# Performance work log

Measured on AMD Instinct MI355X. Metric: run time of the kernel, lower is better.

Reference implementation:

```python
import jax, jax.numpy as jnp
import numpy as np

A, R = 180, 180  # numAngle, numRho
EPS = 1e-5


def _hough_seg_ids(H, W):
    # Deep Hough Transform binning (Hanqer/deep-hough-transform initTab):
    # irho = int(sqrt(H^2+W^2)+1)/(numRho-1); theta_k = k*pi/numAngle
    irho = int(np.sqrt(H * H + W * W) + 1) / float(R - 1)
    theta = np.arange(A) * (np.pi / A)
    tab_cos = np.cos(theta) / irho  # [A]
    tab_sin = np.sin(theta) / irho
    xs = np.arange(W) - W // 2  # x is width index
    ys = np.arange(H) - H // 2
    r = np.round(tab_cos[:, None, None] * xs[None, None, :]
                 + tab_sin[:, None, None] * ys[None, :, None]).astype(np.int64) + R // 2
    r = np.clip(r, 0, R - 1)
    return jnp.asarray(r.reshape(A, H * W))  # [A, H*W] rho-bin per (angle, pixel)


def _conv_bn_relu(x, w, b, g, beta, m, v, pad):
    y = jax.lax.conv_general_dilated(
        x, w, window_strides=(1, 1), padding=[(pad, pad), (pad, pad)],
        dimension_numbers=('NCHW', 'OIHW', 'NCHW'))
    y = y + b[None, :, None, None]
    scale = g / jnp.sqrt(v + EPS)
    y = (y - m[None, :, None, None]) * scale[None, :, None, None] + beta[None, :, None, None]
    return jax.nn.relu(y)


def _dht(f):
    # f: [N, C, H, W] -> accum [N, C, A, R]
    N, C, H, W = f.shape
    seg = _hough_seg_ids(H, W)  # [A, HW]
    ft = f.reshape(N, C, H * W).transpose(2, 0, 1).reshape(H * W, N * C)  # [HW, N*C]
    acc = jax.vmap(lambda s: jax.ops.segment_sum(ft, s, num_segments=R))(seg)  # [A, R, N*C]
    return acc.reshape(A, R, N, C).transpose(2, 3, 0, 1)  # [N, C, A, R]


def setup_inputs() -> dict:
    key = jax.random.key(0)
    ks = jax.random.split(key, 24)
    N, Ci, dim, H, W = 8, 256, 128, 128, 128
    inp = {
        'x': jax.random.normal(ks[0], (N, Ci, H, W), jnp.float32),
        'w1': jax.random.normal(ks[1], (dim, Ci, 1, 1), jnp.float32) * (1.0 / np.sqrt(Ci)),
        'b1': jax.random.normal(ks[2], (dim,), jnp.float32) * 0.01,
        'g1': jax.random.uniform(ks[3], (dim,), jnp.float32, 0.5, 1.5),
        'be1': jax.random.normal(ks[4], (dim,), jnp.float32) * 0.01,
        'm1': jax.random.normal(ks[5], (dim,), jnp.float32) * 0.1,
        'v1': jax.random.uniform(ks[6], (dim,), jnp.float32, 0.5, 1.5),
        'w2': jax.random.normal(ks[7], (dim, dim, 3, 3), jnp.float32) * (1.0 / np.sqrt(dim * 9)),
        'b2': jax.random.normal(ks[8], (dim,), jnp.float32) * 0.01,
        'g2': jax.random.uniform(ks[9], (dim,), jnp.float32, 0.5, 1.5),
        'be2': jax.random.normal(ks[10], (dim,), jnp.float32) * 0.01,
        'm2': jax.random.normal(ks[11], (dim,), jnp.float32) * 0.1,
        'v2': jax.random.uniform(ks[12], (dim,), jnp.float32, 0.5, 1.5),
        'w3': jax.random.normal(ks[13], (dim, dim, 3, 3), jnp.float32) * (1.0 / np.sqrt(dim * 9)),
        'b3': jax.random.normal(ks[14], (dim,), jnp.float32) * 0.01,
        'g3': jax.random.uniform(ks[15], (dim,), jnp.float32, 0.5, 1.5),
        'be3': jax.random.normal(ks[16], (dim,), jnp.float32) * 0.01,
        'm3': jax.random.normal(ks[17], (dim,), jnp.float32) * 0.1,
        'v3': jax.random.uniform(ks[18], (dim,), jnp.float32, 0.5, 1.5),
    }
    return inp


def reference(x, w1, b1, g1, be1, m1, v1,
              w2, b2, g2, be2, m2, v2,
              w3, b3, g3, be3, m3, v3):
    f = _conv_bn_relu(x, w1, b1, g1, be1, m1, v1, pad=0)   # 1x1 conv + BN + ReLU
    acc = _dht(f)                                           # [N, dim, A, R]
    y = _conv_bn_relu(acc, w2, b2, g2, be2, m2, v2, pad=1)  # 3x3 conv + BN + ReLU
    y = _conv_bn_relu(y, w3, b3, g3, be3, m3, v3, pad=1)
    return y
```

## Files before the change

### kernel.cpp

```cpp
#include <hip/hip_runtime.h>
#include <hip/hip_bf16.h>
#include <math.h>

#define NB 8
#define CI 256
#define CD 128
#define HH 128
#define WW 128
#define HW (HH*WW)
#define AANG 180
#define RRHO 180
#define PADD 182
#define M2 (AANG*RRHO)

typedef __attribute__((ext_vector_type(8))) short short8;
typedef __attribute__((ext_vector_type(8))) _Float16 half8;
typedef __attribute__((ext_vector_type(2))) _Float16 h2;
typedef __attribute__((ext_vector_type(4))) float floatx4;
typedef __attribute__((ext_vector_type(2))) float floatx2;

static __device__ __forceinline__ void async_cp16(const void* g, void* l) {
  __builtin_amdgcn_global_load_lds((const __attribute__((address_space(1))) unsigned int*)g,
                                   (__attribute__((address_space(3))) unsigned int*)l,
                                   16, 0, 0);
}

static __device__ __forceinline__ unsigned short f2bf(float f) {
  unsigned int u = __builtin_bit_cast(unsigned int, f);
  unsigned int r = (u + 0x7fffu + ((u >> 16) & 1u)) >> 16;
  return (unsigned short)r;
}

static __device__ __forceinline__ unsigned short f2h(float f) {
  return __builtin_bit_cast(unsigned short, (_Float16)f);
}

static __device__ __forceinline__ void acc2(float& aL, float& aH, unsigned int u,
                                            h2 eL, h2 eH) {
  h2 hv = __builtin_bit_cast(h2, u);
#if __has_builtin(__builtin_amdgcn_fdot2)
  aL = __builtin_amdgcn_fdot2(hv, eL, aL, false);
  aH = __builtin_amdgcn_fdot2(hv, eH, aH, false);
#else
  aL += (float)hv.x;
  aH += (float)hv.y;
#endif
}

__global__ void prep_kernel(const float* __restrict__ w1, const float* __restrict__ w2,
                            const float* __restrict__ w3,
                            const float* b1, const float* g1, const float* be1,
                            const float* m1, const float* v1,
                            const float* b2, const float* g2, const float* be2,
                            const float* m2, const float* v2,
                            const float* b3, const float* g3, const float* be3,
                            const float* m3, const float* v3,
                            unsigned short* __restrict__ wK1, unsigned short* __restrict__ wK2,
                            unsigned short* __restrict__ wK3,
                            float* __restrict__ sc, float* __restrict__ sh) {
  int idx = blockIdx.x * 256 + threadIdx.x;
  if (idx < 32768) {
    wK1[idx] = f2h(w1[idx]);
  } else if (idx < 32768 + 147456) {
    int i = idx - 32768;
    int co = i / 1152, k = i % 1152;
    int dydx = k >> 7, ci = k & 127;
    int dst = (((dydx*2 + (ci >> 6)) * 128 + co) * 64) + (ci & 63);
    wK2[dst] = f2bf(w2[(size_t)(co*128 + ci)*9 + dydx]);
  } else if (idx < 32768 + 2*147456) {
    int i = idx - 32768 - 147456;
    int co = i / 1152, k = i % 1152;
    int dydx = k >> 7, ci = k & 127;
    int dst = (((dydx*2 + (ci >> 6)) * 128 + co) * 64) + (ci & 63);
    wK3[dst] = f2bf(w3[(size_t)(co*128 + ci)*9 + dydx]);
  } else if (idx < 32768 + 2*147456 + 384) {
    int j = idx - 32768 - 2*147456;
    int c = j >> 7, co = j & 127;
    const float* b  = c==0?b1 :(c==1?b2 :b3);
    const float* g  = c==0?g1 :(c==1?g2 :g3);
    const float* be = c==0?be1:(c==1?be2:be3);
    const float* m  = c==0?m1 :(c==1?m2 :m3);
    const float* v  = c==0?v1 :(c==1?v2 :v3);
    float s = g[co] * rsqrtf(v[co] + 1e-5f);
    sc[c*128 + co] = s;
    sh[c*128 + co] = (b[co] - m[co]) * s + be[co];
  }
}

__global__ void hist_kernel(unsigned char* __restrict__ seg, unsigned int* __restrict__ offs) {
  int a = blockIdx.x, t = threadIdx.x;
  __shared__ unsigned int h[RRHO];
  if (t < RRHO) h[t] = 0;
  __syncthreads();
  double th = (double)a * (M_PI / 180.0);
  double Cc = cos(th) / (182.0 / 179.0);
  double Ss = sin(th) / (182.0 / 179.0);
  for (int p = t; p < HW; p += 256) {
    int x = (p & 127) - 64;
    int y = (p >> 7) - 64;
    int r = (int)rint(Cc * (double)x + Ss * (double)y) + 90;
    r = r < 0 ? 0 : (r > 179 ? 179 : r);
    seg[(size_t)a*HW + p] = (unsigned char)r;
    atomicAdd(&h[r], 1u);
  }
  __syncthreads();
  if (t == 0) {
    unsigned int run = 0;
    for (int r = 0; r < RRHO; ++r) { offs[a*192 + r] = run; run += h[r]; }
    offs[a*192 + RRHO] = run;
  }
}

__global__ void fill_kernel(const unsigned char* __restrict__ seg,
                            const unsigned int* __restrict__ offs,
                            unsigned short* __restrict__ lst16) {
  int a = blockIdx.x, t = threadIdx.x;
  __shared__ unsigned int pos[RRHO];
  if (t < RRHO) pos[t] = offs[a*192 + t];
  __syncthreads();
  int p0 = t * 64;
  for (int i = 0; i < 64; ++i) {
    int p = p0 + i;
    int r = seg[(size_t)a*HW + p];
    unsigned int ix = atomicAdd(&pos[r], 1u);
    lst16[(size_t)a*HW + ix] = (unsigned short)p;
  }
}

__global__ void zero_border(uint4* __restrict__ accP, uint4* __restrict__ y2P,
                            unsigned int* __restrict__ qcnt) {
  int idx = blockIdx.x * 256 + threadIdx.x;
  if (idx < 8) qcnt[idx] = 0;
  if (idx >= NB * PADD * PADD) return;
  int rc = idx % (PADD * PADD);
  int row = rc / PADD, col = rc % PADD;
  if (row != 0 && row != PADD-1 && col != 0 && col != PADD-1) return;
  uint4 z = {0u, 0u, 0u, 0u};
  size_t base = (size_t)idx * 16;
  #pragma unroll
  for (int i = 0; i < 16; ++i) { accP[base + i] = z; y2P[base + i] = z; }
}

__global__ __launch_bounds__(256) void conv1_kernel(
    const float* __restrict__ x, const unsigned short* __restrict__ wK,
    const float* __restrict__ sc, const float* __restrict__ sh,
    unsigned short* __restrict__ f) {
  __shared__ short Al[4*128*8];
  __shared__ short Bl[4*128*8];
  int t = threadIdx.x;
  int m0 = blockIdx.x * 128;
  int n = blockIdx.y;
  int lane = t & 63, wv = t >> 6, wm = wv & 1, wn = wv >> 1;
  int mloc = t & 127, octb = t >> 7;
  floatx4 acc[4][4];
  #pragma unroll
  for (int i = 0; i < 4; ++i)
    #pragma unroll
    for (int j = 0; j < 4; ++j) acc[i][j] = (floatx4){0.f, 0.f, 0.f, 0.f};
  const float* xn = x + (size_t)n * CI * HW;
  for (int kc = 0; kc < 8; ++kc) {
    if (kc) __syncthreads();
    #pragma unroll
    for (int j = 0; j < 2; ++j) {
      int oct = octb + 2*j;
      const float* src = xn + (size_t)(kc*32 + oct*8) * HW + m0 + mloc;
      float v[8];
      #pragma unroll
      for (int e = 0; e < 8; ++e) v[e] = src[(size_t)e * HW];
      uint4 pk;
      pk.x = __builtin_bit_cast(unsigned int, __builtin_amdgcn_cvt_pkrtz(v[0], v[1]));
      pk.y = __builtin_bit_cast(unsigned int, __builtin_amdgcn_cvt_pkrtz(v[2], v[3]));
      pk.z = __builtin_bit_cast(unsigned int, __builtin_amdgcn_cvt_pkrtz(v[4], v[5]));
      pk.w = __builtin_bit_cast(unsigned int, __builtin_amdgcn_cvt_pkrtz(v[6], v[7]));
      *reinterpret_cast<uint4*>(&Al[(size_t)(t + 256*j) * 8]) = pk;
    }
    #pragma unroll
    for (int j = 0; j < 2; ++j) {
      int oct = octb + 2*j;
      async_cp16(wK + (size_t)mloc * 256 + kc*32 + oct*8,
                 &Bl[(size_t)((t & 0xFFC0) + 256*j) * 8]);
    }
    __syncthreads();
    int q = lane >> 4, l15 = lane & 15;
    short8 af[4], bfr[4];
    #pragma unroll
    for (int i = 0; i < 4; ++i)
      af[i] = *reinterpret_cast<const short8*>(&Al[((q*128) + wm*64 + i*16 + l15) * 8]);
    #pragma unroll
    for (int j = 0; j < 4; ++j)
      bfr[j] = *reinterpret_cast<const short8*>(&Bl[((q*128) + wn*64 + j*16 + l15) * 8]);
    #pragma unroll
    for (int i = 0; i < 4; ++i)
      #pragma unroll
      for (int j = 0; j < 4; ++j)
        acc[i][j] = __builtin_amdgcn_mfma_f32_16x16x32_f16(
            __builtin_bit_cast(half8, af[i]), __builtin_bit_cast(half8, bfr[j]),
            acc[i][j], 0, 0, 0);
  }
  int q = lane >> 4, l15 = lane & 15;
  #pragma unroll
  for (int j = 0; j < 4; ++j) {
    int co = wn*64 + j*16 + l15;
    float s = sc[co], hb = sh[co];
    #pragma unroll
    for (int i = 0; i < 4; ++i) {
      #pragma unroll
      for (int rg = 0; rg < 4; ++rg) {
        int m = m0 + wm*64 + i*16 + q*4 + rg;
        float v = acc[i][j][rg] * s + hb;
        v = fmaxf(v, 0.f);
        f[((size_t)n * HW + m) * 128 + co] = f2h(v);
      }
    }
  }
}

__global__ __launch_bounds__(512, 8) void dht_kernel(
    const unsigned short* __restrict__ lst16, const unsigned int* __restrict__ offs,
    const unsigned int* __restrict__ f, unsigned int* __restrict__ accP,
    unsigned int* __restrict__ qcnt) {
  __shared__ unsigned short Ls[HW];
  __shared__ unsigned int Os[RRHO + 1];
  __shared__ int sWork;
  int t = threadIdx.x;
  if (t == 0) {
    unsigned int xcd;
    asm volatile("s_getreg_b32 %0, hwreg(HW_REG_XCC_ID, 0, 32)" : "=s"(xcd));
    xcd &= 7u;
    int work = 0;
    for (int k = 0; k < 8; ++k) {
      unsigned int q = (xcd + (unsigned int)k) & 7u;
      unsigned int tk = atomicAdd(&qcnt[q], 1u);
      if (tk < 360u) { work = (int)(q * 360u + tk); break; }
    }
    sWork = work;
  }
  __syncthreads();
  int work = sWork;
  int n = work / 360;
  int rem = work % 360;
  int h = rem / 180;
  int a = rem % 180;
  {
    const uint4* src = (const uint4*)(lst16 + (size_t)a * HW);
    uint4* dst = (uint4*)Ls;
    if (t < RRHO + 1) Os[t] = offs[a*192 + t];
    #pragma unroll
    for (int i = 0; i < 4; ++i) dst[t + 512*i] = src[t + 512*i];
  }
  __syncthreads();
  int w = t >> 6, lane = t & 63;
  int sub = lane >> 3;
  int co  = lane & 7;
  const char* fb = (const char*)(f + (size_t)n * HW * 64);
  unsigned int loff = (unsigned int)(h*32 + co*4) * 4u;
  const h2 eL = {(_Float16)1.0f, (_Float16)0.0f};
  const h2 eH = {(_Float16)0.0f, (_Float16)1.0f};
  for (int r = w; r < RRHO; r += 8) {
    int o0 = (int)Os[r];
    int cnt = (int)Os[r+1] - o0;
    float accL[4], accH[4];
    #pragma unroll
    for (int j = 0; j < 4; ++j) { accL[j] = 0.f; accH[j] = 0.f; }
    int i = 0;
    for (; i + 32 <= cnt; i += 32) {
      unsigned int p0 = Ls[o0 + i + sub];
      unsigned int p1 = Ls[o0 + i + 8 + sub];
      unsigned int p2 = Ls[o0 + i + 16 + sub];
      unsigned int p3 = Ls[o0 + i + 24 + sub];
      uint4 v0 = *(const uint4*)(fb + ((p0 << 8) + loff));
      uint4 v1 = *(const uint4*)(fb + ((p1 << 8) + loff));
      uint4 v2 = *(const uint4*)(fb + ((p2 << 8) + loff));
      uint4 v3 = *(const uint4*)(fb + ((p3 << 8) + loff));
      const unsigned int u0[4] = {v0.x, v0.y, v0.z, v0.w};
      const unsigned int u1[4] = {v1.x, v1.y, v1.z, v1.w};
      const unsigned int u2[4] = {v2.x, v2.y, v2.z, v2.w};
      const unsigned int u3[4] = {v3.x, v3.y, v3.z, v3.w};
      #pragma unroll
      for (int j = 0; j < 4; ++j) {
        acc2(accL[j], accH[j], u0[j], eL, eH);
        acc2(accL[j], accH[j], u1[j], eL, eH);
        acc2(accL[j], accH[j], u2[j], eL, eH);
        acc2(accL[j], accH[j], u3[j], eL, eH);
      }
    }
    for (; i + 8 <= cnt; i += 8) {
      unsigned int p0 = Ls[o0 + i + sub];
      uint4 v0 = *(const uint4*)(fb + ((p0 << 8) + loff));
      const unsigned int u0[4] = {v0.x, v0.y, v0.z, v0.w};
      #pragma unroll
      for (int j = 0; j < 4; ++j)
        acc2(accL[j], accH[j], u0[j], eL, eH);
    }
    if (i < cnt) {
      int idx = i + sub;
      int cl = idx < cnt ? idx : (cnt - 1);
      unsigned int p0 = Ls[o0 + cl];
      uint4 v0 = *(const uint4*)(fb + ((p0 << 8) + loff));
      unsigned int u0[4] = {v0.x, v0.y, v0.z, v0.w};
      if (idx >= cnt) { u0[0] = 0; u0[1] = 0; u0[2] = 0; u0[3] = 0; }
      #pragma unroll
      for (int j = 0; j < 4; ++j)
        acc2(accL[j], accH[j], u0[j], eL, eH);
    }
    #pragma unroll
    for (int m = 8; m <= 32; m <<= 1) {
      #pragma unroll
      for (int j = 0; j < 4; ++j) {
        accL[j] += __shfl_xor(accL[j], m, 64);
        accH[j] += __shfl_xor(accH[j], m, 64);
      }
    }
    if (sub == 0) {
      uint4 out;
      out.x = (unsigned int)f2bf(accL[0]) | ((unsigned int)f2bf(accH[0]) << 16);
      out.y = (unsigned int)f2bf(accL[1]) | ((unsigned int)f2bf(accH[1]) << 16);
      out.z = (unsigned int)f2bf(accL[2]) | ((unsigned int)f2bf(accH[2]) << 16);
      out.w = (unsigned int)f2bf(accL[3]) | ((unsigned int)f2bf(accH[3]) << 16);
      size_t o = (((size_t)n*PADD + (a+1))*PADD + (r+1))*64 + h*32 + co*4;
      *(uint4*)(accP + o) = out;
    }
  }
}

template<int MODE>
__global__ __launch_bounds__(256) void conv3x3_kernel(
    const unsigned short* __restrict__ inP,
    const unsigned short* __restrict__ wKr,
    const float* __restrict__ sc, const float* __restrict__ sh,
    void* __restrict__ outp) {
  __shared__ short Al[128*64];
  __shared__ short Bl[128*64];
  int t = threadIdx.x;
  int m0 = blockIdx.x * 128;
  int n = blockIdx.y;
  int lane = t & 63, w = t >> 6, wm = w & 1, wn = w >> 1;
  floatx4 acc[4][4];
  #pragma unroll
  for (int i = 0; i < 4; ++i)
    #pragma unroll
    for (int j = 0; j < 4; ++j) acc[i][j] = (floatx4){0.f, 0.f, 0.f, 0.f};

  int srcOct = ((lane & 7) - (lane >> 3)) & 7;
  const unsigned short* rpA[4];
  unsigned int offB[4];
  #pragma unroll
  for (int i = 0; i < 4; ++i) {
    int row = w*32 + i*8 + (lane >> 3);
    int mg = m0 + row; if (mg > M2 - 1) mg = M2 - 1;
    int oa = mg / 180, orr = mg % 180;
    rpA[i] = inP + (((size_t)n*PADD + oa)*PADD + orr)*128 + srcOct*8;
    offB[i] = (unsigned int)(row*64 + srcOct*8);
  }

  for (int step = 0; step < 18; ++step) {
    int dydx = step >> 1, cc2 = step & 1;
    int dy = (dydx * 11) >> 5, dx = dydx - dy*3;
    int doff = (dy*PADD + dx)*128 + cc2*64;
    if (step) __syncthreads();
    #pragma unroll
    for (int i = 0; i < 4; ++i) {
      async_cp16(rpA[i] + doff, &Al[(size_t)((w*4 + i)*64 + lane) * 8]);
      async_cp16(wKr + (size_t)step*8192 + offB[i],
                 &Bl[(size_t)((w*4 + i)*64 + lane) * 8]);
    }
    __syncthreads();
    int q = lane >> 4, l15 = lane & 15;
    #pragma unroll
    for (int kk = 0; kk < 2; ++kk) {
      int o = kk*4 + q;
      int swz = ((o + l15) & 7) * 8;
      short8 rf[4], cf[4];
      #pragma unroll
      for (int i = 0; i < 4; ++i) {
        int addr = (wm*64 + i*16 + l15)*64 + swz;
        rf[i] = *reinterpret_cast<const short8*>(MODE == 1 ? &Al[addr] : &Bl[addr]);
      }
      #pragma unroll
      for (int j = 0; j < 4; ++j) {
        int addr = (wn*64 + j*16 + l15)*64 + swz;
        cf[j] = *reinterpret_cast<const short8*>(MODE == 1 ? &Bl[addr] : &Al[addr]);
      }
      #pragma unroll
      for (int i = 0; i < 4; ++i)
        #pragma unroll
        for (int j = 0; j < 4; ++j)
          acc[i][j] = __builtin_amdgcn_mfma_f32_16x16x32_bf16(rf[i], cf[j], acc[i][j], 0, 0, 0);
    }
  }
  int q = lane >> 4, l15 = lane & 15;
  if (MODE == 1) {
    unsigned short* out = (unsigned short*)outp;
    #pragma unroll
    for (int j = 0; j < 4; ++j) {
      int co = wn*64 + j*16 + l15;
      float s = sc[co], hb = sh[co];
      #pragma unroll
      for (int i = 0; i < 4; ++i) {
        #pragma unroll
        for (int rg = 0; rg < 4; ++rg) {
          int m = m0 + wm*64 + i*16 + q*4 + rg;
          if (m < M2) {
            float v = fmaxf(acc[i][j][rg] * s + hb, 0.f);
            int oa2 = m / 180, or2 = m % 180;
            out[(((size_t)n*PADD + oa2 + 1)*PADD + or2 + 1)*128 + co] = f2bf(v);
          }
        }
      }
    }
  } else {
    float* out = (float*)outp;
    #pragma unroll
    for (int i = 0; i < 4; ++i) {
      #pragma unroll
      for (int rg = 0; rg < 4; ++rg) {
        int co = wm*64 + i*16 + q*4 + rg;
        float s = sc[co], hb = sh[co];
        #pragma unroll
        for (int j = 0; j < 4; ++j) {
          int m = m0 + wn*64 + j*16 + l15;
          if (m < M2) {
            float v = fmaxf(acc[i][j][rg] * s + hb, 0.f);
            out[((size_t)n*128 + co)*M2 + m] = v;
          }
        }
      }
    }
  }
}

extern "C" void kernel_launch(void* const* d_in, const int* in_sizes, int n_in,
                              void* d_out, int out_size, void* d_ws, size_t ws_size,
                              hipStream_t stream) {
  const float* x  = (const float*)d_in[0];
  const float* w1 = (const float*)d_in[1];
  const float* b1 = (const float*)d_in[2];
  const float* g1 = (const float*)d_in[3];
  const float* be1= (const float*)d_in[4];
  const float* m1 = (const float*)d_in[5];
  const float* v1 = (const float*)d_in[6];
  const float* w2 = (const float*)d_in[7];
  const float* b2 = (const float*)d_in[8];
  const float* g2 = (const float*)d_in[9];
  const float* be2= (const float*)d_in[10];
  const float* m2 = (const float*)d_in[11];
  const float* v2 = (const float*)d_in[12];
  const float* w3 = (const float*)d_in[13];
  const float* b3 = (const float*)d_in[14];
  const float* g3 = (const float*)d_in[15];
  const float* be3= (const float*)d_in[16];
  const float* m3 = (const float*)d_in[17];
  const float* v3 = (const float*)d_in[18];

  size_t off = 0;
  char* ws = (char*)d_ws;
  auto alloc = [&](size_t sz) -> void* {
    void* p = ws + off;
    off = (off + sz + 255) & ~(size_t)255;
    return p;
  };
  unsigned short* fbuf = (unsigned short*)alloc((size_t)NB*HW*128*2);
  unsigned short* accP = (unsigned short*)alloc((size_t)NB*PADD*PADD*128*2);
  unsigned short* y2P  = (unsigned short*)alloc((size_t)NB*PADD*PADD*128*2);
  unsigned short* wK1  = (unsigned short*)alloc(32768*2);
  unsigned short* wK2  = (unsigned short*)alloc(147456*2);
  unsigned short* wK3  = (unsigned short*)alloc(147456*2);
  float* sc = (float*)alloc(384*4);
  float* sh = (float*)alloc(384*4);
  unsigned char* seg  = (unsigned char*)alloc((size_t)AANG*HW);
  unsigned int* offs  = (unsigned int*)alloc((size_t)AANG*192*4);
  unsigned short* lst16 = (unsigned short*)alloc((size_t)AANG*HW*2);
  unsigned int* qcnt  = (unsigned int*)alloc(8*4);

  prep_kernel<<<1282, 256, 0, stream>>>(w1, w2, w3,
      b1, g1, be1, m1, v1, b2, g2, be2, m2, v2, b3, g3, be3, m3, v3,
      wK1, wK2, wK3, sc, sh);
  hist_kernel<<<AANG, 256, 0, stream>>>(seg, offs);
  fill_kernel<<<AANG, 256, 0, stream>>>(seg, offs, lst16);
  zero_border<<<(NB*PADD*PADD + 255)/256, 256, 0, stream>>>((uint4*)accP, (uint4*)y2P, qcnt);
  conv1_kernel<<<dim3(HW/128, NB), 256, 0, stream>>>(x, wK1, sc, sh, fbuf);
  dht_kernel<<<NB*AANG*2, 512, 0, stream>>>(lst16, offs, (const unsigned int*)fbuf,
                                            (unsigned int*)accP, qcnt);
  conv3x3_kernel<1><<<dim3((M2 + 127)/128, NB), 256, 0, stream>>>(
      accP, wK2, sc + 128, sh + 128, y2P);
  conv3x3_kernel<2><<<dim3((M2 + 127)/128, NB), 256, 0, stream>>>(
      y2P, wK3, sc + 256, sh + 256, d_out);
}
```

Measured before the change: 747.9 us.

## Double-buffer conv3x3 LDS loads and widen Hough gather unroll

The conv3x3 kernel now double-buffers its A and B tiles in LDS. It issues the async global-to-LDS copy for the next K step before computing the current one, using explicit vmcnt waits and barriers, so load latency overlaps with MFMA work. The Hough gather loop now processes 64 entries per iteration, taking 32 from each end of the segment, to keep more global loads in flight. In exchange, the conv kernel uses twice the LDS (64KB), which may reduce occupancy, and the code depends on hand-written waitcnt counts being correct.

```diff
diff --git a/kernel.cpp b/kernel.cpp
--- a/kernel.cpp
+++ b/kernel.cpp
@@ -45,6 +45,14 @@
   aL += (float)hv.x;
   aH += (float)hv.y;
 #endif
+}
+
+static __device__ __forceinline__ void acc4(float* aL, float* aH, const uint4& v,
+                                            h2 eL, h2 eH) {
+  acc2(aL[0], aH[0], v.x, eL, eH);
+  acc2(aL[1], aH[1], v.y, eL, eH);
+  acc2(aL[2], aH[2], v.z, eL, eH);
+  acc2(aL[3], aH[3], v.w, eL, eH);
 }
 
 __global__ void prep_kernel(const float* __restrict__ w1, const float* __restrict__ w2,
@@ -257,51 +265,58 @@
   const h2 eL = {(_Float16)1.0f, (_Float16)0.0f};
   const h2 eH = {(_Float16)0.0f, (_Float16)1.0f};
   for (int r = w; r < RRHO; r += 8) {
-    int o0 = (int)Os[r];
-    int cnt = (int)Os[r+1] - o0;
+    int lo = (int)Os[r];
+    int hi = (int)Os[r+1];
     float accL[4], accH[4];
     #pragma unroll
     for (int j = 0; j < 4; ++j) { accL[j] = 0.f; accH[j] = 0.f; }
-    int i = 0;
-    for (; i + 32 <= cnt; i += 32) {
-      unsigned int p0 = Ls[o0 + i + sub];
-      unsigned int p1 = Ls[o0 + i + 8 + sub];
-      unsigned int p2 = Ls[o0 + i + 16 + sub];
-      unsigned int p3 = Ls[o0 + i + 24 + sub];
+    while (hi - lo >= 64) {
+      unsigned int p0 = Ls[lo + sub];
+      unsigned int p1 = Ls[lo + 8 + sub];
+      unsigned int p2 = Ls[lo + 16 + sub];
+      unsigned int p3 = Ls[lo + 24 + sub];
+      unsigned int p4 = Ls[hi - 32 + sub];
+      unsigned int p5 = Ls[hi - 24 + sub];
+      unsigned int p6 = Ls[hi - 16 + sub];
+      unsigned int p7 = Ls[hi - 8 + sub];
       uint4 v0 = *(const uint4*)(fb + ((p0 << 8) + loff));
       uint4 v1 = *(const uint4*)(fb + ((p1 << 8) + loff));
       uint4 v2 = *(const uint4*)(fb + ((p2 << 8) + loff));
       uint4 v3 = *(const uint4*)(fb + ((p3 << 8) + loff));
-      const unsigned int u0[4] = {v0.x, v0.y, v0.z, v0.w};
-      const unsigned int u1[4] = {v1.x, v1.y, v1.z, v1.w};
-      const unsigned int u2[4] = {v2.x, v2.y, v2.z, v2.w};
-      const unsigned int u3[4] = {v3.x, v3.y, v3.z, v3.w};
-      #pragma unroll
-      for (int j = 0; j < 4; ++j) {
-        acc2(accL[j], accH[j], u0[j], eL, eH);
-        acc2(accL[j], accH[j], u1[j], eL, eH);
-        acc2(accL[j], accH[j], u2[j], eL, eH);
-        acc2(accL[j], accH[j], u3[j], eL, eH);
-      }
-    }
-    for (; i + 8 <= cnt; i += 8) {
-      unsigned int p0 = Ls[o0 + i + sub];
+      uint4 v4 = *(const uint4*)(fb + ((p4 << 8) + loff));
+      uint4 v5 = *(const uint4*)(fb + ((p5 << 8) + loff));
+      uint4 v6 = *(const uint4*)(fb + ((p6 << 8) + loff));
+      uint4 v7 = *(const uint4*)(fb + ((p7 << 8) + loff));
+      acc4(accL, accH, v0, eL, eH); acc4(accL, accH, v1, eL, eH);
+      acc4(accL, accH, v2, eL, eH); acc4(accL, accH, v3, eL, eH);
+      acc4(accL, accH, v4, eL, eH); acc4(accL, accH, v5, eL, eH);
+      acc4(accL, accH, v6, eL, eH); acc4(accL, accH, v7, eL, eH);
+      lo += 32; hi -= 32;
+    }
+    for (; lo + 32 <= hi; lo += 32) {
+      unsigned int p0 = Ls[lo + sub];
+      unsigned int p1 = Ls[lo + 8 + sub];
+      unsigned int p2 = Ls[lo + 16 + sub];
+      unsigned int p3 = Ls[lo + 24 + sub];
       uint4 v0 = *(const uint4*)(fb + ((p0 << 8) + loff));
-      const unsigned int u0[4] = {v0.x, v0.y, v0.z, v0.w};
-      #pragma unroll
-      for (int j = 0; j < 4; ++j)
-        acc2(accL[j], accH[j], u0[j], eL, eH);
-    }
-    if (i < cnt) {
-      int idx = i + sub;
-      int cl = idx < cnt ? idx : (cnt - 1);
-      unsigned int p0 = Ls[o0 + cl];
+      uint4 v1 = *(const uint4*)(fb + ((p1 << 8) + loff));
+      uint4 v2 = *(const uint4*)(fb + ((p2 << 8) + loff));
+      uint4 v3 = *(const uint4*)(fb + ((p3 << 8) + loff));
+      acc4(accL, accH, v0, eL, eH); acc4(accL, accH, v1, eL, eH);
+      acc4(accL, accH, v2, eL, eH); acc4(accL, accH, v3, eL, eH);
+    }
+    for (; lo + 8 <= hi; lo += 8) {
+      unsigned int p0 = Ls[lo + sub];
       uint4 v0 = *(const uint4*)(fb + ((p0 << 8) + loff));
-      unsigned int u0[4] = {v0.x, v0.y, v0.z, v0.w};
-      if (idx >= cnt) { u0[0] = 0; u0[1] = 0; u0[2] = 0; u0[3] = 0; }
-      #pragma unroll
-      for (int j = 0; j < 4; ++j)
-        acc2(accL[j], accH[j], u0[j], eL, eH);
+      acc4(accL, accH, v0, eL, eH);
+    }
+    if (lo < hi) {
+      int idx = lo + sub;
+      int cl = idx < hi ? idx : (hi - 1);
+      unsigned int p0 = Ls[cl];
+      uint4 v0 = *(const uint4*)(fb + ((p0 << 8) + loff));
+      if (idx >= hi) { v0.x = 0; v0.y = 0; v0.z = 0; v0.w = 0; }
+      acc4(accL, accH, v0, eL, eH);
     }
     #pragma unroll
     for (int m = 8; m <= 32; m <<= 1) {
@@ -329,8 +344,8 @@
     const unsigned short* __restrict__ wKr,
     const float* __restrict__ sc, const float* __restrict__ sh,
     void* __restrict__ outp) {
-  __shared__ short Al[128*64];
-  __shared__ short Bl[128*64];
+  __shared__ short Al[2][128*64];
+  __shared__ short Bl[2][128*64];
   int t = threadIdx.x;
   int m0 = blockIdx.x * 128;
   int n = blockIdx.y;
@@ -353,18 +368,18 @@
     offB[i] = (unsigned int)(row*64 + srcOct*8);
   }
 
-  for (int step = 0; step < 18; ++step) {
+  auto stage = [&](int step, int b) {
     int dydx = step >> 1, cc2 = step & 1;
     int dy = (dydx * 11) >> 5, dx = dydx - dy*3;
     int doff = (dy*PADD + dx)*128 + cc2*64;
-    if (step) __syncthreads();
     #pragma unroll
     for (int i = 0; i < 4; ++i) {
-      async_cp16(rpA[i] + doff, &Al[(size_t)((w*4 + i)*64 + lane) * 8]);
+      async_cp16(rpA[i] + doff, &Al[b][(size_t)((w*4 + i)*64 + lane) * 8]);
       async_cp16(wKr + (size_t)step*8192 + offB[i],
-                 &Bl[(size_t)((w*4 + i)*64 + lane) * 8]);
-    }
-    __syncthreads();
+                 &Bl[b][(size_t)((w*4 + i)*64 + lane) * 8]);
+    }
+  };
+  auto compute = [&](int b) {
     int q = lane >> 4, l15 = lane & 15;
     #pragma unroll
     for (int kk = 0; kk < 2; ++kk) {
@@ -374,12 +389,12 @@
       #pragma unroll
       for (int i = 0; i < 4; ++i) {
         int addr = (wm*64 + i*16 + l15)*64 + swz;
-        rf[i] = *reinterpret_cast<const short8*>(MODE == 1 ? &Al[addr] : &Bl[addr]);
+        rf[i] = *reinterpret_cast<const short8*>(MODE == 1 ? &Al[b][addr] : &Bl[b][addr]);
       }
       #pragma unroll
       for (int j = 0; j < 4; ++j) {
         int addr = (wn*64 + j*16 + l15)*64 + swz;
-        cf[j] = *reinterpret_cast<const short8*>(MODE == 1 ? &Bl[addr] : &Al[addr]);
+        cf[j] = *reinterpret_cast<const short8*>(MODE == 1 ? &Bl[b][addr] : &Al[b][addr]);
       }
       #pragma unroll
       for (int i = 0; i < 4; ++i)
@@ -387,7 +402,31 @@
         for (int j = 0; j < 4; ++j)
           acc[i][j] = __builtin_amdgcn_mfma_f32_16x16x32_bf16(rf[i], cf[j], acc[i][j], 0, 0, 0);
     }
-  }
+  };
+
+  stage(0, 0);
+  #pragma unroll 1
+  for (int s2 = 0; s2 < 9; ++s2) {
+    stage(2*s2 + 1, 1);
+    asm volatile("s_waitcnt vmcnt(8)" ::: "memory");
+    __builtin_amdgcn_s_barrier();
+    __builtin_amdgcn_sched_barrier(0);
+    compute(0);
+    asm volatile("s_waitcnt lgkmcnt(0)" ::: "memory");
+    __builtin_amdgcn_s_barrier();
+    if (s2 < 8) {
+      stage(2*s2 + 2, 0);
+      asm volatile("s_waitcnt vmcnt(8)" ::: "memory");
+    } else {
+      asm volatile("s_waitcnt vmcnt(0)" ::: "memory");
+    }
+    __builtin_amdgcn_s_barrier();
+    __builtin_amdgcn_sched_barrier(0);
+    compute(1);
+    asm volatile("s_waitcnt lgkmcnt(0)" ::: "memory");
+    __builtin_amdgcn_s_barrier();
+  }
+
   int q = lane >> 4, l15 = lane & 15;
   if (MODE == 1) {
     unsigned short* out = (unsigned short*)outp;
```

New measurement: 790.8 us. +5.7%, slower.
